# Kernel tuning notes

Hardware: AMD Instinct MI355X
Metric: run time of the kernel (lower is better)

Reference implementation:

```python
import jax, jax.numpy as jnp
import numpy as np
from jax import lax

BASE = 10000.0

def _rope(x):
    # x: (b, h, w, c). Faithful to torch RoPE: angles depend only on one spatial
    # axis (h,k_max) and broadcast against the *w* axis of x (valid since h==w).
    b, h, w, c = x.shape
    k_max = c // 2
    theta = 1.0 / (BASE ** (jnp.arange(k_max, dtype=x.dtype) / k_max))  # (k_max,)
    angles = jnp.arange(h, dtype=x.dtype)[:, None] * theta              # (h, k_max)
    cos = jnp.cos(angles)[None, None]  # (1,1,h,k_max) -> broadcasts over w axis
    sin = jnp.sin(angles)[None, None]
    xr = x.reshape(b, h, w, k_max, 2)
    re, im = xr[..., 0], xr[..., 1]
    out = jnp.stack([re * cos - im * sin, re * sin + im * cos], axis=-1)
    return out.reshape(b, h, w, c)


def setup_inputs() -> dict:
    key = jax.random.key(0)
    k1, k2, k3 = jax.random.split(key, 3)
    B, C, H, W = 8, 128, 160, 160
    x = jax.random.normal(k1, (B, C, H, W), dtype=jnp.float32)
    qk_w = jax.random.normal(k2, (2 * C, C), dtype=jnp.float32) * 0.02
    qk_b = jnp.zeros((2 * C,), dtype=jnp.float32)
    lepe_w = jax.random.normal(k3, (C, 1, 3, 3), dtype=jnp.float32) * 0.1
    lepe_b = jnp.zeros((C,), dtype=jnp.float32)
    return {"x": x, "qk_w": qk_w, "qk_b": qk_b,
            "lepe_w": lepe_w, "lepe_b": lepe_b, "num_heads": 8}


def reference(x, qk_w, qk_b, lepe_w, lepe_b, num_heads):
    b, c, H, W = x.shape
    n = H * W
    hd = c // num_heads
    # raw row-major reshape (B,C,H,W) -> (B,N,C), matching torch .reshape
    xf = x.reshape(b, n, c)
    qk = (xf @ qk_w.T + qk_b).reshape(b, n, 2, c)
    q = jax.nn.elu(qk[:, :, 0]) + 1.0
    k = jax.nn.elu(qk[:, :, 1]) + 1.0
    v = xf
    q_rope = _rope(q.reshape(b, H, W, c)).reshape(b, n, num_heads, hd).transpose(0, 2, 1, 3)
    k_rope = _rope(k.reshape(b, H, W, c)).reshape(b, n, num_heads, hd).transpose(0, 2, 1, 3)
    qh = q.reshape(b, n, num_heads, hd).transpose(0, 2, 1, 3)  # (b,h,n,d)
    kh = k.reshape(b, n, num_heads, hd).transpose(0, 2, 1, 3)
    vh = v.reshape(b, n, num_heads, hd).transpose(0, 2, 1, 3)
    z = 1.0 / (jnp.einsum('bhnd,bhd->bhn', qh, kh.mean(axis=2)) + 1e-6)  # (b,h,n)
    scale = float(n) ** -0.5
    kv = jnp.einsum('bhnd,bhne->bhde', k_rope * scale, vh * scale)  # (b,h,d,d)
    out = jnp.einsum('bhnd,bhde->bhne', q_rope, kv) * z[..., None]  # (b,h,n,d)
    out = out.transpose(0, 2, 1, 3).reshape(b, n, c)
    # LePE: depthwise 3x3 conv on v laid out as image
    vimg = vh.transpose(0, 2, 1, 3).reshape(b, H, W, c).transpose(0, 3, 1, 2)  # (b,c,H,W)
    lepe = lax.conv_general_dilated(vimg, lepe_w, (1, 1), 'SAME',
                                    feature_group_count=c)
    lepe = lepe + lepe_b[None, :, None, None]
    out = out + lepe.transpose(0, 2, 3, 1).reshape(b, n, c)
    return out.transpose(0, 2, 1).reshape(b, c, H, W)
```

## Files before the change

### kernel.cpp

```cpp
#include <hip/hip_runtime.h>
#include <cstdint>
#include <cstddef>

#define NB 8
#define NC 128
#define NHH 160
#define NWW 160
#define NNN (NHH*NWW)
#define TILE_R 64
#define TPB (NNN/TILE_R)
#define NSLOTS 32
#define LN_B 0.14391156511f

typedef __attribute__((ext_vector_type(8))) short short8v;
typedef __attribute__((ext_vector_type(4))) short short4v;
typedef __attribute__((ext_vector_type(4))) float f32x4;
union B64x2 { short8v v8; short4v v4[2]; ushort u[8]; uint w[4]; };

__device__ __forceinline__ float elup1(float y){ return y>0.f? y+1.f : __expf(y); }
__device__ __forceinline__ ushort f2bf(float f){ uint x=__float_as_uint(f); x+=0x7fffu+((x>>16)&1u); return (ushort)(x>>16); }
__device__ __forceinline__ uint cvtpk(float lo, float hi){
  uint r;
  asm("v_cvt_pk_bf16_f32 %0, %1, %2" : "=v"(r) : "v"(lo), "v"(hi));
  return r;
}
__device__ __forceinline__ float frcp(float x){
  float r;
  asm("v_rcp_f32 %0, %1" : "=v"(r) : "v"(x));
  return r;
}
__device__ __forceinline__ float bfhi(uint u){ return __uint_as_float(u & 0xffff0000u); }
__device__ __forceinline__ float bflo(uint u){ return __uint_as_float(u << 16); }
__device__ __forceinline__ int divH(int i){ return ((i >> 5) * 6554) >> 15; }
__device__ __forceinline__ int iclamp(int v, int lo, int hi){ return v<lo?lo:(v>hi?hi:v); }

__global__ __launch_bounds__(256) void kprep(
    const float* __restrict__ qk_w, ushort* __restrict__ wbf,
    float2* __restrict__ rtab, float* __restrict__ zreg)
{
  const int id = blockIdx.x*256 + threadIdx.x;
  if (id < 2*NC*NC) wbf[id] = f2bf(qk_w[id]);
  if (id < NWW*64) {
    const int ww = id >> 6, f = id & 63;
    const float th = __expf(-LN_B * (float)f);
    float s, c; __sincosf((float)ww * th, &s, &c);
    rtab[id] = make_float2(c, s);
  }
  #pragma unroll
  for (int j = 0; j < 17; ++j)
    zreg[id + j*32768] = 0.f;
}

__global__ __launch_bounds__(256, 3) void k1_proj(
    const float* __restrict__ x, const ushort* __restrict__ wbf,
    const float* __restrict__ qk_b, const float2* __restrict__ rtab,
    ushort* __restrict__ qu, float* __restrict__ kv_part,
    float* __restrict__ ksum_part)
{
  __shared__ __align__(16) ushort xbf[64][136];
  __shared__ __align__(16) ushort wch[64][136];
  __shared__ float ksum_lds[NC];
  ushort* xtp = &wch[0][0];
  ushort* krt = &wch[0][0] + 4352;

  const int blk  = ((blockIdx.x & 7) * (NB*TPB/8)) + (blockIdx.x >> 3);
  const int b    = blk / TPB;
  const int tile = blk - b * TPB;
  const int i0   = tile * TILE_R;
  const int tid  = threadIdx.x;
  const int lane = tid & 63;
  const int wv   = tid >> 6;
  const int lg   = lane >> 4;
  const int ll   = lane & 15;
  const float* xb = x + (size_t)b*NNN*NC + (size_t)i0*NC;

  {
    const float4* src = (const float4*)xb;
    for (int f = tid; f < TILE_R*NC/4; f += 256) {
      float4 v = src[f];
      uint w0 = cvtpk(v.x, v.y), w1 = cvtpk(v.z, v.w);
      *(uint2*)&xbf[f >> 5][(f & 31) << 2] = make_uint2(w0, w1);
    }
  }
  if (tid < NC) ksum_lds[tid] = 0.f;

  f32x4 kvacc[2];
  kvacc[0] = (f32x4){0.f,0.f,0.f,0.f};
  kvacc[1] = (f32x4){0.f,0.f,0.f,0.f};
  const int row0 = (wv<<4) + (lg<<2);

  int wfr4[4];
  #pragma unroll
  for (int r = 0; r < 4; ++r) {
    const int i = i0 + row0 + r;
    wfr4[r] = i - divH(i)*NWW;
  }

  for (int chunk = 0; chunk < 4; ++chunk) {
    if (chunk) __syncthreads();
    {
      const uint4* wsrc = (const uint4*)(wbf + (size_t)(chunk*64)*NC);
      for (int f = tid; f < 1024; f += 256)
        *(uint4*)&wch[f >> 4][(f & 15) << 3] = wsrc[f];
    }
    __syncthreads();

    f32x4 acc[4];
    acc[0]=acc[1]=acc[2]=acc[3]=(f32x4){0.f,0.f,0.f,0.f};
    #pragma unroll
    for (int ks = 0; ks < 4; ++ks) {
      short8v a = *(const short8v*)&xbf[(wv<<4) + ll][(ks<<5) + (lg<<3)];
      #pragma unroll
      for (int nt = 0; nt < 4; ++nt) {
        short8v bb = *(const short8v*)&wch[(nt<<4) + ll][(ks<<5) + (lg<<3)];
        acc[nt] = __builtin_amdgcn_mfma_f32_16x16x32_bf16(a, bb, acc[nt], 0, 0, 0);
      }
    }

    if (chunk < 2) {
      ushort* qb = qu + ((size_t)b*NNN + (size_t)i0)*NC;
      #pragma unroll
      for (int nt = 0; nt < 4; ++nt) {
        const int cg = (chunk<<6) + (nt<<4) + ll;
        const float bias = qk_b[cg];
        #pragma unroll
        for (int r = 0; r < 4; ++r)
          qb[(size_t)(row0 + r)*NC + cg] = f2bf(elup1(acc[nt][r] + bias));
      }
    } else {
      uint rbw[4][2];
      #pragma unroll
      for (int nt = 0; nt < 4; ++nt) {
        const int kc = ((chunk-2)<<6) + (nt<<4) + ll;
        const float bias = qk_b[NC + kc];
        float kk[4]; float ss = 0.f;
        #pragma unroll
        for (int r = 0; r < 4; ++r) { kk[r] = elup1(acc[nt][r] + bias); ss += kk[r]; }
        atomicAdd(&ksum_lds[kc], ss);
        ushort rb[4];
        #pragma unroll
        for (int r = 0; r < 4; ++r) {
          float p = __shfl_xor(kk[r], 1);
          float2 cs = rtab[wfr4[r]*64 + (kc >> 1)];
          float kr = (kc & 1) ? (p*cs.y + kk[r]*cs.x) : (kk[r]*cs.x - p*cs.y);
          rb[r] = f2bf(kr);
        }
        rbw[nt][0] = (uint)rb[0] | ((uint)rb[1] << 16);
        rbw[nt][1] = (uint)rb[2] | ((uint)rb[3] << 16);
      }
      __syncthreads();

      #pragma unroll
      for (int nt = 0; nt < 4; ++nt) {
        const int kcl = (nt<<4) + ll;
        *(uint*)&krt[kcl*68 + row0]     = rbw[nt][0];
        *(uint*)&krt[kcl*68 + row0 + 2] = rbw[nt][1];
      }
      #pragma unroll
      for (int t = 0; t < 2; ++t) {
        const int task = tid + (t << 8);
        const int c = task & 63, rg = task >> 6;
        ushort tmp[8];
        #pragma unroll
        for (int k2 = 0; k2 < 8; ++k2) tmp[k2] = xbf[(rg<<3)+k2][((chunk-2)<<6)+c];
        *(ushort4*)&xtp[c*68 + (rg<<3)]     = make_ushort4(tmp[0],tmp[1],tmp[2],tmp[3]);
        *(ushort4*)&xtp[c*68 + (rg<<3) + 4] = make_ushort4(tmp[4],tmp[5],tmp[6],tmp[7]);
      }
      __syncthreads();

      const int e2 = chunk - 2;
      #pragma unroll
      for (int ks = 0; ks < 2; ++ks) {
        const int rb2 = (ks<<5) + (lg<<3);
        B64x2 ua, ub;
        ua.v4[0] = *(const short4v*)&krt[((wv<<4) + ll)*68 + rb2];
        ua.v4[1] = *(const short4v*)&krt[((wv<<4) + ll)*68 + rb2 + 4];
        ub.v4[0] = *(const short4v*)&xtp[((wv<<4) + ll)*68 + rb2];
        ub.v4[1] = *(const short4v*)&xtp[((wv<<4) + ll)*68 + rb2 + 4];
        kvacc[e2] = __builtin_amdgcn_mfma_f32_16x16x32_bf16(ua.v8, ub.v8, kvacc[e2], 0, 0, 0);
      }
    }
  }

  const int slot = blk & (NSLOTS-1);
  {
    float* kvp = kv_part + ((size_t)b*NSLOTS + slot) * 2048;
    #pragma unroll
    for (int e2 = 0; e2 < 2; ++e2) {
      const int h = (e2<<2) + wv;
      #pragma unroll
      for (int r = 0; r < 4; ++r) {
        const int d = (lg<<2) + r;
        atomicAdd(&kvp[(h<<8) + (d<<4) + ll], kvacc[e2][r]);
      }
    }
  }
  __syncthreads();
  if (tid < NC) atomicAdd(&ksum_part[((size_t)b*NSLOTS + slot)*NC + tid], ksum_lds[tid]);
}

__global__ __launch_bounds__(256) void k_reduce(
    const float* __restrict__ kv_part, const float* __restrict__ ksum_part,
    float* __restrict__ kvf, float* __restrict__ kmean)
{
  const int gtid = blockIdx.x * 256 + threadIdx.x;
  const int b = gtid >> 11;
  const int cidx = gtid & 2047;
  float s = 0.f;
  for (int sl = 0; sl < NSLOTS; ++sl)
    s += kv_part[((size_t)b*NSLOTS + sl)*2048 + cidx];
  kvf[(size_t)b*2048 + cidx] = s * (1.f/25600.f);
  if (cidx < NC) {
    float t = 0.f;
    for (int sl = 0; sl < NSLOTS; ++sl)
      t += ksum_part[((size_t)b*NSLOTS + sl)*NC + cidx];
    kmean[(size_t)b*NC + cidx] = t * (1.f/25600.f);
  }
}

__global__ __launch_bounds__(256, 2) void k2_out(
    const float* __restrict__ x, const ushort* __restrict__ qu,
    const float* __restrict__ kvf, const float* __restrict__ kmean,
    const float* __restrict__ lepe_w, const float* __restrict__ lepe_b,
    const float2* __restrict__ rtab, float* __restrict__ outp)
{
  __shared__ __align__(16) ushort qu_s[64*136];

  const int blk  = ((blockIdx.x & 7) * (NB*TPB/8)) + (blockIdx.x >> 3);
  const int b    = blk / TPB;
  const int tile = blk - b * TPB;
  const int i0   = tile * TILE_R;
  const int tid  = threadIdx.x;
  const int lane = tid & 63;
  const int wv   = tid >> 6;
  const int lg   = lane >> 4;
  const int ll   = lane & 15;
  const float* xb = x + (size_t)b*NNN*NC;

  {
    const uint4* qsrc = (const uint4*)(qu + ((size_t)b*NNN + (size_t)i0)*NC);
    #pragma unroll
    for (int t = 0; t < 4; ++t) {
      const int f = tid + (t << 8);
      uint4 v = qsrc[f];
      const int row = f >> 4, c8 = f & 15;
      *(uint4*)&qu_s[row*136 + ((c8 ^ (row & 7)) << 3)] = v;
    }
  }
  __syncthreads();

  const bool interior = (i0 >= 192) && (i0 <= NNN - 225);

  int wfa[4];
  #pragma unroll
  for (int mt = 0; mt < 4; ++mt) {
    const int i = i0 + (mt<<4) + ll;
    wfa[mt] = i - divH(i)*NWW;
  }

  #pragma unroll
  for (int hs = 0; hs < 2; ++hs) {
    const int h  = wv + (hs<<2);
    const int ch = (h<<4) + ll;
    B64x2 kb, kz;
    kb.v8 = (short8v){0,0,0,0,0,0,0,0};
    kz.v8 = (short8v){0,0,0,0,0,0,0,0};
    if (lg < 2) {
      const float* kvp = kvf + (size_t)b*2048 + (h<<8) + ll;
      #pragma unroll
      for (int j2 = 0; j2 < 4; ++j2) {
        float f0 = kvp[(((lg<<3) + 2*j2    ) << 4)];
        float f1 = kvp[(((lg<<3) + 2*j2 + 1) << 4)];
        kb.w[j2] = cvtpk(f0, f1);
      }
      const float* kmp = kmean + (size_t)b*NC + (h<<4) + (lg<<3);
      #pragma unroll
      for (int j2 = 0; j2 < 4; ++j2)
        kz.w[j2] = cvtpk(kmp[2*j2], kmp[2*j2+1]);
    }
    f32x4 pacc[4], zacc[4];
    #pragma unroll
    for (int mt = 0; mt < 4; ++mt) {
      short8v a  = (short8v){0,0,0,0,0,0,0,0};
      short8v au = (short8v){0,0,0,0,0,0,0,0};
      if (lg < 2) {
        const int row = (mt<<4) + ll;
        const int off = row*136 + ((((h<<1) + lg) ^ (row & 7)) << 3);
        B64x2 uq;
        uq.v8 = *(const short8v*)&qu_s[off];
        au = uq.v8;
        const float2* tp = rtab + wfa[mt]*64 + (h<<3) + (lg<<2);
        B64x2 ra;
        #pragma unroll
        for (int j = 0; j < 4; ++j) {
          float2 cs = tp[j];
          float e = bflo(uq.w[j]), o = bfhi(uq.w[j]);
          ra.w[j] = cvtpk(e*cs.x - o*cs.y, e*cs.y + o*cs.x);
        }
        a = ra.v8;
      }
      pacc[mt] = __builtin_amdgcn_mfma_f32_16x16x32_bf16(
          a,  kb.v8, (f32x4){0.f,0.f,0.f,0.f}, 0, 0, 0);
      zacc[mt] = __builtin_amdgcn_mfma_f32_16x16x32_bf16(
          au, kz.v8, (f32x4){0.f,0.f,0.f,0.f}, 0, 0, 0);
    }
    float wl[9];
    #pragma unroll
    for (int t = 0; t < 9; ++t) wl[t] = lepe_w[ch*9 + t];
    const float lb = lepe_b[ch];
    const float* xc = xb + ch;

    if (interior) {
      #pragma unroll
      for (int mt = 0; mt < 4; ++mt) {
        const int lrow = (mt<<4) + (lg<<2);
        const int ib   = i0 + lrow;
        const float* pu = xc + (size_t)(ib-161)*NC;
        const float* pm = xc + (size_t)(ib-1  )*NC;
        const float* pd = xc + (size_t)(ib+159)*NC;
        float mu[6], mm[6], md[6];
        #pragma unroll
        for (int j = 0; j < 6; ++j) {
          mu[j] = pu[j*NC]; mm[j] = pm[j*NC]; md[j] = pd[j*NC];
        }
        int ww = ib - divH(ib)*NWW;
        float4 ov;
        #pragma unroll
        for (int r = 0; r < 4; ++r) {
          const float zz = frcp(zacc[mt][r] + 1e-6f);
          const float fx0 = ww > 0   ? 1.f : 0.f;
          const float fx2 = ww < 159 ? 1.f : 0.f;
          float lp = lb;
          lp += fx0*(wl[0]*mu[r] + wl[3]*mm[r] + wl[6]*md[r]);
          lp +=     (wl[1]*mu[r+1] + wl[4]*mm[r+1] + wl[7]*md[r+1]);
          lp += fx2*(wl[2]*mu[r+2] + wl[5]*mm[r+2] + wl[8]*md[r+2]);
          (&ov.x)[r] = pacc[mt][r]*zz + lp;
          ww = (ww == NWW-1) ? 0 : ww + 1;
        }
        *(float4*)(outp + ((size_t)b*NC + ch)*NNN + ib) = ov;
      }
    } else {
      #pragma unroll
      for (int mt = 0; mt < 4; ++mt) {
        const int lrow = (mt<<4) + (lg<<2);
        const int ib   = i0 + lrow;
        float mu[6], mm[6], md[6];
        #pragma unroll
        for (int j = 0; j < 6; ++j) {
          const int im = ib - 1 + j;
          mu[j] = xc[(size_t)(iclamp(im-160, 0, NNN-1)) * NC];
          mm[j] = xc[(size_t)(iclamp(im,     0, NNN-1)) * NC];
          md[j] = xc[(size_t)(iclamp(im+160, 0, NNN-1)) * NC];
        }
        int hh = divH(ib);
        int ww = ib - hh*NWW;
        float4 ov;
        #pragma unroll
        for (int r = 0; r < 4; ++r) {
          const float zz = frcp(zacc[mt][r] + 1e-6f);
          const float fy0 = hh > 0   ? 1.f : 0.f;
          const float fy2 = hh < 159 ? 1.f : 0.f;
          const float fx0 = ww > 0   ? 1.f : 0.f;
          const float fx2 = ww < 159 ? 1.f : 0.f;
          float lp = lb;
          lp += fy0*(fx0*wl[0]*mu[r] + wl[1]*mu[r+1] + fx2*wl[2]*mu[r+2]);
          lp +=     (fx0*wl[3]*mm[r] + wl[4]*mm[r+1] + fx2*wl[5]*mm[r+2]);
          lp += fy2*(fx0*wl[6]*md[r] + wl[7]*md[r+1] + fx2*wl[8]*md[r+2]);
          (&ov.x)[r] = pacc[mt][r]*zz + lp;
          const int cy = (ww == NWW-1) ? 1 : 0;
          hh += cy;
          ww = cy ? 0 : ww + 1;
        }
        *(float4*)(outp + ((size_t)b*NC + ch)*NNN + ib) = ov;
      }
    }
  }
}

extern "C" void kernel_launch(void* const* d_in, const int* in_sizes, int n_in,
                              void* d_out, int out_size, void* d_ws, size_t ws_size,
                              hipStream_t stream) {
  const float* x      = (const float*)d_in[0];
  const float* qk_w   = (const float*)d_in[1];
  const float* qk_b   = (const float*)d_in[2];
  const float* lepe_w = (const float*)d_in[3];
  const float* lepe_b = (const float*)d_in[4];
  float* outp = (float*)d_out;

  float* kv_part   = (float*)d_ws;
  float* ksum_part = kv_part + (size_t)NB*NSLOTS*2048;
  float* kvf       = ksum_part + (size_t)NB*NSLOTS*NC;
  float* kmean     = kvf + (size_t)NB*2048;
  float2* rtab     = (float2*)(kmean + (size_t)NB*NC);
  ushort* wbf      = (ushort*)(rtab + (size_t)NWW*64);
  ushort* qubuf    = wbf + (size_t)2*NC*NC;

  hipLaunchKernelGGL(kprep, dim3(128), dim3(256), 0, stream,
                     qk_w, wbf, rtab, kv_part);
  hipLaunchKernelGGL(k1_proj, dim3(NB*TPB), dim3(256), 0, stream,
                     x, wbf, qk_b, rtab, qubuf, kv_part, ksum_part);
  hipLaunchKernelGGL(k_reduce, dim3(64), dim3(256), 0, stream,
                     kv_part, ksum_part, kvf, kmean);
  hipLaunchKernelGGL(k2_out, dim3(NB*TPB), dim3(256), 0, stream,
                     x, qubuf, kvf, kmean, lepe_w, lepe_b, rtab, outp);
}
```

Baseline: 157.2 us.

## Prefetch weight chunks into registers and store Q in MFMA-fragment order

The projection kernel now loads the next 64-row weight chunk into registers while the current chunk is computed, so global loads overlap the MFMA work instead of running just before it. The intermediate Q buffer is written in MFMA accumulator layout, as packed bf16 pairs in coalesced 8-byte stores, replacing scattered 2-byte stores. The output kernel reads that layout back coalesced and scatters it into its swizzled LDS tile with 2-byte shared stores. This trades extra register pressure and more LDS store instructions in the second kernel for fewer, wider global transactions.

Result: slower. 178.8 us (+13.8%).

```diff
diff --git a/kernel.cpp b/kernel.cpp
--- a/kernel.cpp
+++ b/kernel.cpp
@@ -73,6 +73,11 @@
   const int lg   = lane >> 4;
   const int ll   = lane & 15;
   const float* xb = x + (size_t)b*NNN*NC + (size_t)i0*NC;
+  const uint4* wsrc = (const uint4*)wbf;
+
+  uint4 wreg[4];
+  #pragma unroll
+  for (int t = 0; t < 4; ++t) wreg[t] = wsrc[tid + (t<<8)];
 
   {
     const float4* src = (const float4*)xb;
@@ -99,9 +104,16 @@
   for (int chunk = 0; chunk < 4; ++chunk) {
     if (chunk) __syncthreads();
     {
-      const uint4* wsrc = (const uint4*)(wbf + (size_t)(chunk*64)*NC);
-      for (int f = tid; f < 1024; f += 256)
-        *(uint4*)&wch[f >> 4][(f & 15) << 3] = wsrc[f];
+      #pragma unroll
+      for (int t = 0; t < 4; ++t) {
+        const int f = tid + (t<<8);
+        *(uint4*)&wch[f >> 4][(f & 15) << 3] = wreg[t];
+      }
+      if (chunk < 3) {
+        #pragma unroll
+        for (int t = 0; t < 4; ++t)
+          wreg[t] = wsrc[((chunk+1)<<10) + tid + (t<<8)];
+      }
     }
     __syncthreads();
 
@@ -118,14 +130,17 @@
     }
 
     if (chunk < 2) {
-      ushort* qb = qu + ((size_t)b*NNN + (size_t)i0)*NC;
+      uint2* qdst = (uint2*)(qu + ((size_t)b*NNN + (size_t)i0)*NC)
+                  + ((size_t)chunk << 10);
       #pragma unroll
       for (int nt = 0; nt < 4; ++nt) {
         const int cg = (chunk<<6) + (nt<<4) + ll;
         const float bias = qk_b[cg];
-        #pragma unroll
-        for (int r = 0; r < 4; ++r)
-          qb[(size_t)(row0 + r)*NC + cg] = f2bf(elup1(acc[nt][r] + bias));
+        float q0 = elup1(acc[nt][0] + bias);
+        float q1 = elup1(acc[nt][1] + bias);
+        float q2 = elup1(acc[nt][2] + bias);
+        float q3 = elup1(acc[nt][3] + bias);
+        qdst[(nt<<8) + tid] = make_uint2(cvtpk(q0, q1), cvtpk(q2, q3));
       }
     } else {
       uint rbw[4][2];
@@ -236,15 +251,22 @@
   const int lg   = lane >> 4;
   const int ll   = lane & 15;
   const float* xb = x + (size_t)b*NNN*NC;
+  const int row0 = (wv<<4) + (lg<<2);
 
   {
-    const uint4* qsrc = (const uint4*)(qu + ((size_t)b*NNN + (size_t)i0)*NC);
+    const uint2* qsrc = (const uint2*)(qu + ((size_t)b*NNN + (size_t)i0)*NC);
     #pragma unroll
-    for (int t = 0; t < 4; ++t) {
-      const int f = tid + (t << 8);
-      uint4 v = qsrc[f];
-      const int row = f >> 4, c8 = f & 15;
-      *(uint4*)&qu_s[row*136 + ((c8 ^ (row & 7)) << 3)] = v;
+    for (int c = 0; c < 2; ++c) {
+      #pragma unroll
+      for (int nt = 0; nt < 4; ++nt) {
+        uint2 v = qsrc[(c<<10) + (nt<<8) + tid];
+        const int cg = (c<<6) + (nt<<4) + ll;
+        const int bsel = cg >> 3, coff = cg & 7;
+        qu_s[(row0+0)*136 + (((bsel) ^ ((row0+0)&7))<<3) + coff] = (ushort)(v.x & 0xffffu);
+        qu_s[(row0+1)*136 + (((bsel) ^ ((row0+1)&7))<<3) + coff] = (ushort)(v.x >> 16);
+        qu_s[(row0+2)*136 + (((bsel) ^ ((row0+2)&7))<<3) + coff] = (ushort)(v.y & 0xffffu);
+        qu_s[(row0+3)*136 + (((bsel) ^ ((row0+3)&7))<<3) + coff] = (ushort)(v.y >> 16);
+      }
     }
   }
   __syncthreads();
```
